# Optimization experiments

Hardware: AMD Instinct MI355X
Metric: run time of the kernel (lower is better)

The kernel has to match this reference:

```python
import jax, jax.numpy as jnp
import numpy as np

K_NN = 8        # neighbors
RADIUS = 0.1    # neighbor distance cutoff


def setup_inputs() -> dict:
    key = jax.random.key(0)
    k1, k2 = jax.random.split(key)
    B, N, KS = 2, 8192, 16  # batch, points, mask slots
    pc = jax.random.uniform(k1, (B, N, 3), dtype=jnp.float32)
    mask = jax.random.uniform(k2, (B, N, KS), dtype=jnp.float32)
    return {"pc": pc, "mask": mask}


def _knn(k, pc):
    # squared pairwise distances via gemm: (B,N,N)
    sq = jnp.sum(pc * pc, axis=-1)
    d2 = sq[:, :, None] + sq[:, None, :] - 2.0 * jnp.einsum("bnd,bmd->bnm", pc, pc)
    d2 = jnp.maximum(d2, 0.0)
    neg_d2, idx = jax.lax.top_k(-d2, k)          # k smallest distances
    dist = jnp.sqrt(jnp.maximum(-neg_d2, 0.0))   # (B,N,k) euclidean
    return dist, idx


def reference(pc, mask):
    # mask: (B,N,KS) -> (B,KS,N)
    mask_t = jnp.transpose(mask, (0, 2, 1))
    dist, idx = _knn(K_NN, pc)                   # (B,N,k) each
    # replace out-of-radius neighbors with the self index (nearest = self)
    self_idx = idx[:, :, :1]                     # (B,N,1)
    idx = jnp.where(dist > RADIUS, self_idx, idx)
    idx = jax.lax.stop_gradient(idx)
    # grouping_operation: (B,KS,N) gathered at (B,N,k) -> (B,KS,N,k)
    nn_mask = jax.vmap(lambda f, i: f[:, i])(mask_t, idx)
    # loss_norm=1: L1 norm over mask-slot dim (dim=1), mean over k, mean overall
    diff = mask_t[:, :, :, None] - nn_mask       # (B,KS,N,k)
    loss = jnp.sum(jnp.abs(diff), axis=1).mean(axis=-1)  # (B,N)
    return loss.mean()
```

## Files before the change

### kernel.cpp

```cpp
#include <hip/hip_runtime.h>

#define BATCH 2
#define NPTS  8192
#define KS    16
#define KNN   8
#define R2LOOSE 0.0101f
#define KEYMASK 0xFFFFE000u
#define NCELL   1000
#define CSTRIDE 1024

#define QB       64
#define NWAVE    8
#define NTHREADS 512
#define CAP      32
#define TILEC    1024
#define NBLK     (BATCH * NPTS / QB)

__device__ __forceinline__ int cell_of(float x, float y, float z) {
    int cx = (int)(x * 10.0f); cx = cx > 9 ? 9 : cx;
    int cy = (int)(y * 10.0f); cy = cy > 9 ? 9 : cy;
    int cz = (int)(z * 10.0f); cz = cz > 9 ? 9 : cz;
    return (cx * 10 + cy) * 10 + cz;
}

__global__ __launch_bounds__(1024) void count_kernel(
    const float* __restrict__ pc, int* __restrict__ hist16) {
    __shared__ int h[1024];
    const int blk = blockIdx.x, t = threadIdx.x;
    h[t] = 0;
    __syncthreads();
    const int i = blk * 1024 + t;
    const float x = pc[3 * i], y = pc[3 * i + 1], z = pc[3 * i + 2];
    atomicAdd(&h[cell_of(x, y, z)], 1);
    __syncthreads();
    hist16[blk * 1024 + t] = h[t];
}

__global__ __launch_bounds__(1024) void scatter_kernel(
    const float* __restrict__ pc, const int* __restrict__ hist16,
    float4* __restrict__ cs, int* __restrict__ sidx,
    int* __restrict__ cstart, float* __restrict__ out) {
    __shared__ int arr[1024];
    const int blk = blockIdx.x, t = threadIdx.x;
    const int b  = blk >> 3;
    const int j0 = b * 8;

    int sum = 0, bel = 0;
#pragma unroll
    for (int j = 0; j < 8; ++j) {
        const int v = hist16[(j0 + j) * 1024 + t];
        sum += v;
        bel += ((j0 + j) < blk) ? v : 0;
    }
    arr[t] = sum;
    __syncthreads();
    for (int off = 1; off < 1024; off <<= 1) {
        const int v = (t >= off) ? arr[t - off] : 0;
        __syncthreads();
        arr[t] += v;
        __syncthreads();
    }
    const int excl = arr[t] - sum;
    if ((blk & 7) == 0) cstart[b * CSTRIDE + t] = excl;
    if (blk == 0 && t == 0) out[0] = 0.0f;
    __syncthreads();
    arr[t] = excl + bel;
    __syncthreads();

    const int i = blk * 1024 + t;
    const float x = pc[3 * i], y = pc[3 * i + 1], z = pc[3 * i + 2];
    const float sq = fmaf(z, z, fmaf(y, y, x * x));
    const int pos = atomicAdd(&arr[cell_of(x, y, z)], 1);
    cs[b * NPTS + pos]   = make_float4(x, y, z, -0.5f * sq);
    sidx[b * NPTS + pos] = i & (NPTS - 1);
}

__global__ __launch_bounds__(512) void knn_loss_kernel(
    const float4* __restrict__ cs,
    const int*    __restrict__ sidx,
    const int*    __restrict__ cstart,
    const float*  __restrict__ mask,
    float* __restrict__ out)
{
    __shared__ float4   tile[TILEC];
    __shared__ int      tsp[TILEC];
    __shared__ unsigned sbuf[CAP * NTHREADS];
    __shared__ int      fidx[QB * KNN];
    __shared__ int      qid[QB];
    __shared__ float    red[NWAVE];

    const int t = threadIdx.x;
    const int q = t & (QB - 1);
    const int s = t >> 6;
    const int su = __builtin_amdgcn_readfirstlane(s);
    const int blk = blockIdx.x;
    const int b  = blk >> 7;
    const int q0 = (blk & 127) * QB;
    const int qpos = q0 + q;

    const float4* csb = cs + b * NPTS;
    const float4 qc = csb[qpos];
    const int    qi = sidx[b * NPTS + qpos];
    if (s == 0) qid[q] = qi;

    const float qx = qc.x, qy = qc.y, qz = qc.z;
    const float qs = -2.0f * qc.w;
    const float negthr = (qs - R2LOOSE) * 0.5f;
    const unsigned SENT = (__float_as_uint(R2LOOSE) & KEYMASK) | 0x1FFFu;

    int lex = cell_of(qx, qy, qz);
    int cmn = lex, cmx = lex;
#pragma unroll
    for (int off = 32; off; off >>= 1) {
        cmn = min(cmn, __shfl_xor(cmn, off));
        cmx = max(cmx, __shfl_xor(cmx, off));
    }
    const int cfirst = __builtin_amdgcn_readfirstlane(cmn);
    const int clast  = __builtin_amdgcn_readfirstlane(cmx);

    int lo0 = cfirst - 111, h0 = clast - 89;
    int lo1 = cfirst - 11,  h1 = clast + 11;
    int lo2 = cfirst + 89,  h2 = clast + 111;
    lo0 = min(max(lo0, 0), 1000);
    lo1 = min(max(lo1, 0), 1000);
    lo2 = min(max(lo2, 0), 1000);
    int hp0 = min(max(h0 + 1, 0), 1000);
    int hp1 = min(max(h1 + 1, 0), 1000);
    int hp2 = min(max(h2 + 1, 0), 1000);
    lo1 = max(lo1, hp0);
    lo2 = max(lo2, hp1);

    const int* csp = cstart + b * CSTRIDE;
    const int P0 = csp[lo0], E0 = csp[hp0];
    const int P1 = csp[lo1], E1 = csp[hp1];
    const int P2 = csp[lo2], E2 = csp[hp2];
    const int L0 = max(0, E0 - P0);
    const int L1 = max(0, E1 - P1);
    const int L2 = max(0, E2 - P2);
    const int C  = L0 + L1 + L2;

    int cnt = 0;
    auto EVAL = [&](const float4& c, int spos) {
        const float tt = fmaf(c.x, qx, fmaf(c.y, qy, fmaf(c.z, qz, c.w)));
        const float d2 = fmaxf(fmaf(-2.0f, tt, qs), 0.0f);
        const unsigned key =
            (__float_as_uint(d2) & KEYMASK) | (unsigned)spos;
        const int slot = cnt < (CAP - 1) ? cnt : (CAP - 1);
        sbuf[slot * NTHREADS + t] = key;
        cnt += (tt >= negthr) ? 1 : 0;
    };

    for (int tb = 0; tb < C; tb += TILEC) {
        const int nt = min(TILEC, C - tb);
        for (int p = t; p < nt; p += NTHREADS) {
            const int g = tb + p;
            int sp = P0 + g;
            sp = (g >= L0)      ? (P1 + (g - L0))      : sp;
            sp = (g >= L0 + L1) ? (P2 + (g - L0 - L1)) : sp;
            tile[p] = csb[sp];
            tsp[p]  = sp;
        }
        __syncthreads();

        int j = (su * nt) >> 3;
        const int e = ((su + 1) * nt) >> 3;
        for (; j + 4 <= e; j += 4) {
            const float4 c0 = tile[j],     c1 = tile[j + 1];
            const float4 c2 = tile[j + 2], c3 = tile[j + 3];
            const int s0 = tsp[j],     s1 = tsp[j + 1];
            const int s2 = tsp[j + 2], s3 = tsp[j + 3];
            EVAL(c0, s0); EVAL(c1, s1); EVAL(c2, s2); EVAL(c3, s3);
        }
        for (; j < e; ++j) { const float4 c0 = tile[j]; EVAL(c0, tsp[j]); }
        __syncthreads();
    }

    unsigned md[KNN];
#pragma unroll
    for (int k = 0; k < KNN; ++k) md[k] = SENT;
    const int m = cnt < CAP ? cnt : CAP;
    for (int k = 0; k < m; ++k) {
        unsigned ky = sbuf[k * NTHREADS + t];
#pragma unroll
        for (int i = 0; i < KNN; ++i) {
            const unsigned mn = min(ky, md[i]);
            const unsigned mx = max(ky, md[i]);
            md[i] = mn; ky = mx;
        }
    }
    __syncthreads();

    {
        uint4* bp = (uint4*)&sbuf[t * KNN];
        bp[0] = make_uint4(md[0], md[1], md[2], md[3]);
        bp[1] = make_uint4(md[4], md[5], md[6], md[7]);
    }
    __syncthreads();

    if (s == 0) {
        for (int l = 1; l < NWAVE; ++l) {
            const uint4* lp = (const uint4*)&sbuf[(l * QB + q) * KNN];
            const uint4 r0 = lp[0], r1 = lp[1];
            const unsigned tk[8] = {r0.x, r0.y, r0.z, r0.w,
                                    r1.x, r1.y, r1.z, r1.w};
#pragma unroll
            for (int k = 0; k < 8; ++k) {
                unsigned ky = tk[k];
                if (ky < md[KNN - 1]) {
#pragma unroll
                    for (int i = 0; i < KNN; ++i) {
                        const unsigned mn = min(ky, md[i]);
                        const unsigned mx = max(ky, md[i]);
                        md[i] = mn; ky = mx;
                    }
                }
            }
        }
#pragma unroll
        for (int k = 0; k < KNN; ++k) {
            const unsigned ky = md[k];
            int nb;
            if (ky >= SENT) {
                nb = qi;
            } else {
                const int sp = (int)(ky & 0x1FFFu);
                const float4 cc = csb[sp];
                const float dx = cc.x - qx;
                const float dy = cc.y - qy;
                const float dz = cc.z - qz;
                const float d2 = fmaf(dx, dx, fmaf(dy, dy, dz * dz));
                nb = (sqrtf(d2) > 0.1f) ? qi : sidx[b * NPTS + sp];
            }
            fidx[q * KNN + k] = nb;
        }
    }
    __syncthreads();

    const int q2 = t >> 3;
    const int j2 = t & 7;
    const int qg = qid[q2];
    const int nb = fidx[q2 * KNN + j2];
    const float* mrow = mask + ((size_t)b * NPTS + qg) * KS;
    const float* nrow = mask + ((size_t)b * NPTS + nb) * KS;
    float acc = 0.0f;
#pragma unroll
    for (int c = 0; c < KS; c += 4) {
        const float4 a = *(const float4*)(mrow + c);
        const float4 v = *(const float4*)(nrow + c);
        acc += fabsf(a.x - v.x) + fabsf(a.y - v.y) +
               fabsf(a.z - v.z) + fabsf(a.w - v.w);
    }

#pragma unroll
    for (int off = 32; off > 0; off >>= 1) acc += __shfl_down(acc, off);
    if ((t & 63) == 0) red[s] = acc;
    __syncthreads();
    if (t == 0) {
        float sum = 0.0f;
#pragma unroll
        for (int i = 0; i < NWAVE; ++i) sum += red[i];
        atomicAdd(out, sum * (1.0f / (BATCH * NPTS * KNN)));
    }
}

extern "C" void kernel_launch(void* const* d_in, const int* in_sizes, int n_in,
                              void* d_out, int out_size, void* d_ws, size_t ws_size,
                              hipStream_t stream) {
    const float* pc   = (const float*)d_in[0];
    const float* mask = (const float*)d_in[1];
    float* out = (float*)d_out;

    float4* cs     = (float4*)d_ws;
    int*    sidx   = (int*)((char*)d_ws + 262144);
    int*    cstart = (int*)((char*)d_ws + 327680);
    int*    hist16 = (int*)((char*)d_ws + 335872);

    hipLaunchKernelGGL(count_kernel,   dim3(16), dim3(1024), 0, stream,
                       pc, hist16);
    hipLaunchKernelGGL(scatter_kernel, dim3(16), dim3(1024), 0, stream,
                       pc, hist16, cs, sidx, cstart, out);
    hipLaunchKernelGGL(knn_loss_kernel, dim3(NBLK), dim3(512), 0, stream,
                       cs, sidx, cstart, mask, out);
}
```

Measured before the change: 79.81 us.

## Replace LDS candidate tiling with register readlane broadcast; use wave-shuffle scan

The KNN candidate loop no longer stages candidate points into shared memory with block barriers. Each wave now loads 64 candidates into registers, prefetching the next batch, and broadcasts each one to all lanes with readlane. Only in-radius candidates write a key to the sort buffer, and that write is now under a branch. The scatter kernel's 1024-wide Hillis-Steele LDS prefix scan, which needed about 20 barriers, becomes a two-level wave-shuffle scan. This removes barriers and LDS traffic, at the cost of scalar readlane work and possible divergence per candidate.

After: 81.75 us. 2.4% more time.

```diff
diff --git a/kernel.cpp b/kernel.cpp
--- a/kernel.cpp
+++ b/kernel.cpp
@@ -13,7 +13,6 @@
 #define NWAVE    8
 #define NTHREADS 512
 #define CAP      32
-#define TILEC    1024
 #define NBLK     (BATCH * NPTS / QB)
 
 __device__ __forceinline__ int cell_of(float x, float y, float z) {
@@ -23,6 +22,14 @@
     return (cx * 10 + cy) * 10 + cz;
 }
 
+__device__ __forceinline__ float bcastf(float v, int j) {
+    return __uint_as_float((unsigned)__builtin_amdgcn_readlane(
+        (int)__float_as_uint(v), j));
+}
+__device__ __forceinline__ int bcasti(int v, int j) {
+    return __builtin_amdgcn_readlane(v, j);
+}
+
 __global__ __launch_bounds__(1024) void count_kernel(
     const float* __restrict__ pc, int* __restrict__ hist16) {
     __shared__ int h[1024];
@@ -40,10 +47,12 @@
     const float* __restrict__ pc, const int* __restrict__ hist16,
     float4* __restrict__ cs, int* __restrict__ sidx,
     int* __restrict__ cstart, float* __restrict__ out) {
-    __shared__ int arr[1024];
+    __shared__ int cur[1024];
+    __shared__ int wsum[16];
     const int blk = blockIdx.x, t = threadIdx.x;
     const int b  = blk >> 3;
     const int j0 = b * 8;
+    const int lane = t & 63, w = t >> 6;
 
     int sum = 0, bel = 0;
 #pragma unroll
@@ -52,25 +61,35 @@
         sum += v;
         bel += ((j0 + j) < blk) ? v : 0;
     }
-    arr[t] = sum;
-    __syncthreads();
-    for (int off = 1; off < 1024; off <<= 1) {
-        const int v = (t >= off) ? arr[t - off] : 0;
-        __syncthreads();
-        arr[t] += v;
-        __syncthreads();
-    }
-    const int excl = arr[t] - sum;
+    int inc = sum;
+#pragma unroll
+    for (int off = 1; off < 64; off <<= 1) {
+        const int v = __shfl_up(inc, off);
+        if (lane >= off) inc += v;
+    }
+    if (lane == 63) wsum[w] = inc;
+    __syncthreads();
+    if (w == 0) {
+        const int v = (lane < 16) ? wsum[lane] : 0;
+        int iv = v;
+#pragma unroll
+        for (int off = 1; off < 16; off <<= 1) {
+            const int u = __shfl_up(iv, off);
+            if (lane >= off) iv += u;
+        }
+        if (lane < 16) wsum[lane] = iv - v;
+    }
+    __syncthreads();
+    const int excl = inc - sum + wsum[w];
     if ((blk & 7) == 0) cstart[b * CSTRIDE + t] = excl;
     if (blk == 0 && t == 0) out[0] = 0.0f;
-    __syncthreads();
-    arr[t] = excl + bel;
+    cur[t] = excl + bel;
     __syncthreads();
 
     const int i = blk * 1024 + t;
     const float x = pc[3 * i], y = pc[3 * i + 1], z = pc[3 * i + 2];
     const float sq = fmaf(z, z, fmaf(y, y, x * x));
-    const int pos = atomicAdd(&arr[cell_of(x, y, z)], 1);
+    const int pos = atomicAdd(&cur[cell_of(x, y, z)], 1);
     cs[b * NPTS + pos]   = make_float4(x, y, z, -0.5f * sq);
     sidx[b * NPTS + pos] = i & (NPTS - 1);
 }
@@ -82,8 +101,6 @@
     const float*  __restrict__ mask,
     float* __restrict__ out)
 {
-    __shared__ float4   tile[TILEC];
-    __shared__ int      tsp[TILEC];
     __shared__ unsigned sbuf[CAP * NTHREADS];
     __shared__ int      fidx[QB * KNN];
     __shared__ int      qid[QB];
@@ -140,39 +157,46 @@
     const int C  = L0 + L1 + L2;
 
     int cnt = 0;
-    auto EVAL = [&](const float4& c, int spos) {
-        const float tt = fmaf(c.x, qx, fmaf(c.y, qy, fmaf(c.z, qz, c.w)));
-        const float d2 = fmaxf(fmaf(-2.0f, tt, qs), 0.0f);
-        const unsigned key =
-            (__float_as_uint(d2) & KEYMASK) | (unsigned)spos;
-        const int slot = cnt < (CAP - 1) ? cnt : (CAP - 1);
-        sbuf[slot * NTHREADS + t] = key;
-        cnt += (tt >= negthr) ? 1 : 0;
-    };
-
-    for (int tb = 0; tb < C; tb += TILEC) {
-        const int nt = min(TILEC, C - tb);
-        for (int p = t; p < nt; p += NTHREADS) {
-            const int g = tb + p;
-            int sp = P0 + g;
-            sp = (g >= L0)      ? (P1 + (g - L0))      : sp;
-            sp = (g >= L0 + L1) ? (P2 + (g - L0 - L1)) : sp;
-            tile[p] = csb[sp];
-            tsp[p]  = sp;
-        }
-        __syncthreads();
-
-        int j = (su * nt) >> 3;
-        const int e = ((su + 1) * nt) >> 3;
-        for (; j + 4 <= e; j += 4) {
-            const float4 c0 = tile[j],     c1 = tile[j + 1];
-            const float4 c2 = tile[j + 2], c3 = tile[j + 3];
-            const int s0 = tsp[j],     s1 = tsp[j + 1];
-            const int s2 = tsp[j + 2], s3 = tsp[j + 3];
-            EVAL(c0, s0); EVAL(c1, s1); EVAL(c2, s2); EVAL(c3, s3);
-        }
-        for (; j < e; ++j) { const float4 c0 = tile[j]; EVAL(c0, tsp[j]); }
-        __syncthreads();
+    {
+        const int vlo = (su * C) >> 3;
+        const int vhi = ((su + 1) * C) >> 3;
+        auto FLAT2SP = [&](int fi) {
+            fi = min(fi, C - 1);
+            int sp = P0 + fi;
+            sp = (fi >= L0)      ? (P1 + (fi - L0))      : sp;
+            sp = (fi >= L0 + L1) ? (P2 + (fi - L0 - L1)) : sp;
+            return sp;
+        };
+        if (vhi > vlo) {
+            int spv = FLAT2SP(vlo + q);
+            float4 c = csb[spv];
+            for (int g = vlo; g < vhi; g += QB) {
+                const int nj = min(QB, vhi - g);
+                const int gn = g + QB;
+                int spn = spv; float4 cn = c;
+                if (gn < vhi) { spn = FLAT2SP(gn + q); cn = csb[spn]; }
+#pragma unroll
+                for (int j = 0; j < QB; ++j) {
+                    if (j >= nj) break;
+                    const float sx = bcastf(c.x, j);
+                    const float sy = bcastf(c.y, j);
+                    const float sz = bcastf(c.z, j);
+                    const float sw = bcastf(c.w, j);
+                    const int  ssp = bcasti(spv, j);
+                    const float tt = fmaf(sx, qx,
+                                     fmaf(sy, qy, fmaf(sz, qz, sw)));
+                    if (tt >= negthr) {
+                        const float d2 = fmaxf(fmaf(-2.0f, tt, qs), 0.0f);
+                        const unsigned key =
+                            (__float_as_uint(d2) & KEYMASK) | (unsigned)ssp;
+                        const int slot = cnt < (CAP - 1) ? cnt : (CAP - 1);
+                        sbuf[slot * NTHREADS + t] = key;
+                        ++cnt;
+                    }
+                }
+                spv = spn; c = cn;
+            }
+        }
     }
 
     unsigned md[KNN];
@@ -244,9 +268,9 @@
     const float* nrow = mask + ((size_t)b * NPTS + nb) * KS;
     float acc = 0.0f;
 #pragma unroll
-    for (int c = 0; c < KS; c += 4) {
-        const float4 a = *(const float4*)(mrow + c);
-        const float4 v = *(const float4*)(nrow + c);
+    for (int c2 = 0; c2 < KS; c2 += 4) {
+        const float4 a = *(const float4*)(mrow + c2);
+        const float4 v = *(const float4*)(nrow + c2);
         acc += fabsf(a.x - v.x) + fabsf(a.y - v.y) +
                fabsf(a.z - v.z) + fabsf(a.w - v.w);
     }
```

## Fuse grid histogram and scatter into one redundant per-batch build kernel

Applied to the files above, without the earlier changes.

Merges the count and scatter kernels into a single kernel. Each of the 8 blocks per batch recomputes the full batch histogram in shared memory and takes its slot offset from ordered per-segment atomics, using a syncthreads between segments. The 1024-entry prefix scan now uses wave shuffles instead of a log-step shared-memory scan. This removes one kernel launch and the global histogram round trip, at the cost of every block reading all 8192 points of its batch and running 8 barrier-separated atomic rounds.

New measurement: 77.44 us (median of 2 runs). 3.0% less time.

```diff
diff --git a/kernel.cpp b/kernel.cpp
--- a/kernel.cpp
+++ b/kernel.cpp
@@ -23,56 +23,73 @@
     return (cx * 10 + cy) * 10 + cz;
 }
 
-__global__ __launch_bounds__(1024) void count_kernel(
-    const float* __restrict__ pc, int* __restrict__ hist16) {
+__global__ __launch_bounds__(1024) void build_kernel(
+    const float* __restrict__ pc,
+    float4* __restrict__ cs, int* __restrict__ sidx,
+    int* __restrict__ cstart, float* __restrict__ out)
+{
     __shared__ int h[1024];
+    __shared__ int wsum[16];
     const int blk = blockIdx.x, t = threadIdx.x;
+    const int b = blk >> 3, seg = blk & 7;
+    const int lane = t & 63, w = t >> 6;
+
     h[t] = 0;
-    __syncthreads();
-    const int i = blk * 1024 + t;
-    const float x = pc[3 * i], y = pc[3 * i + 1], z = pc[3 * i + 2];
-    atomicAdd(&h[cell_of(x, y, z)], 1);
-    __syncthreads();
-    hist16[blk * 1024 + t] = h[t];
-}
-
-__global__ __launch_bounds__(1024) void scatter_kernel(
-    const float* __restrict__ pc, const int* __restrict__ hist16,
-    float4* __restrict__ cs, int* __restrict__ sidx,
-    int* __restrict__ cstart, float* __restrict__ out) {
-    __shared__ int arr[1024];
-    const int blk = blockIdx.x, t = threadIdx.x;
-    const int b  = blk >> 3;
-    const int j0 = b * 8;
-
-    int sum = 0, bel = 0;
+    if (blk == 0 && t == 0) out[0] = 0.0f;
+
+    const float* p = pc + (size_t)b * NPTS * 3;
+    float X[8], Y[8], Z[8]; int CC[8];
 #pragma unroll
     for (int j = 0; j < 8; ++j) {
-        const int v = hist16[(j0 + j) * 1024 + t];
-        sum += v;
-        bel += ((j0 + j) < blk) ? v : 0;
-    }
-    arr[t] = sum;
-    __syncthreads();
-    for (int off = 1; off < 1024; off <<= 1) {
-        const int v = (t >= off) ? arr[t - off] : 0;
+        const int i = j * 1024 + t;
+        X[j] = p[3 * i]; Y[j] = p[3 * i + 1]; Z[j] = p[3 * i + 2];
+        CC[j] = cell_of(X[j], Y[j], Z[j]);
+    }
+    __syncthreads();
+
+    int myold = 0;
+#pragma unroll
+    for (int j = 0; j < 8; ++j) {
+        const int old = atomicAdd(&h[CC[j]], 1);
+        if (j == seg) myold = old;
         __syncthreads();
-        arr[t] += v;
-        __syncthreads();
-    }
-    const int excl = arr[t] - sum;
-    if ((blk & 7) == 0) cstart[b * CSTRIDE + t] = excl;
-    if (blk == 0 && t == 0) out[0] = 0.0f;
-    __syncthreads();
-    arr[t] = excl + bel;
-    __syncthreads();
-
-    const int i = blk * 1024 + t;
-    const float x = pc[3 * i], y = pc[3 * i + 1], z = pc[3 * i + 2];
-    const float sq = fmaf(z, z, fmaf(y, y, x * x));
-    const int pos = atomicAdd(&arr[cell_of(x, y, z)], 1);
-    cs[b * NPTS + pos]   = make_float4(x, y, z, -0.5f * sq);
-    sidx[b * NPTS + pos] = i & (NPTS - 1);
+    }
+
+    const int sum = h[t];
+    int inc = sum;
+#pragma unroll
+    for (int off = 1; off < 64; off <<= 1) {
+        const int v = __shfl_up(inc, off);
+        if (lane >= off) inc += v;
+    }
+    if (lane == 63) wsum[w] = inc;
+    __syncthreads();
+    if (w == 0) {
+        const int v = (lane < 16) ? wsum[lane] : 0;
+        int iv = v;
+#pragma unroll
+        for (int off = 1; off < 16; off <<= 1) {
+            const int u = __shfl_up(iv, off);
+            if (lane >= off) iv += u;
+        }
+        if (lane < 16) wsum[lane] = iv - v;
+    }
+    __syncthreads();
+    const int excl = inc - sum + wsum[w];
+    if (seg == 0) cstart[b * CSTRIDE + t] = excl;
+    __syncthreads();
+    h[t] = excl;
+    __syncthreads();
+
+    float mx = X[0], my_ = Y[0], mz = Z[0]; int mc = CC[0];
+#pragma unroll
+    for (int j = 1; j < 8; ++j)
+        if (seg == j) { mx = X[j]; my_ = Y[j]; mz = Z[j]; mc = CC[j]; }
+
+    const int pos = h[mc] + myold;
+    const float sq = fmaf(mz, mz, fmaf(my_, my_, mx * mx));
+    cs[b * NPTS + pos]   = make_float4(mx, my_, mz, -0.5f * sq);
+    sidx[b * NPTS + pos] = seg * 1024 + t;
 }
 
 __global__ __launch_bounds__(512) void knn_loss_kernel(
@@ -273,12 +290,9 @@
     float4* cs     = (float4*)d_ws;
     int*    sidx   = (int*)((char*)d_ws + 262144);
     int*    cstart = (int*)((char*)d_ws + 327680);
-    int*    hist16 = (int*)((char*)d_ws + 335872);
-
-    hipLaunchKernelGGL(count_kernel,   dim3(16), dim3(1024), 0, stream,
-                       pc, hist16);
-    hipLaunchKernelGGL(scatter_kernel, dim3(16), dim3(1024), 0, stream,
-                       pc, hist16, cs, sidx, cstart, out);
+
+    hipLaunchKernelGGL(build_kernel, dim3(16), dim3(1024), 0, stream,
+                       pc, cs, sidx, cstart, out);
     hipLaunchKernelGGL(knn_loss_kernel, dim3(NBLK), dim3(512), 0, stream,
                        cs, sidx, cstart, mask, out);
 }
```
